# Optimization experiments

Hardware: AMD Instinct MI355X
Metric: run time of the kernel (lower is better)

## Reference

```python
import jax, jax.numpy as jnp
import numpy as np

NEG = -9999.0      # chart init / clip floor (np.clip a_min=-9999.0)
THRESH = -9000.0   # 'pseudo_score > -9000' acceptance gate
ARC_BONUS = 5.0    # '+ 5' added to every arc candidate


def _fill_chart(vinfo):
    """Eisner DP chart fill, faithful to the sequential numpy triple loop.
    vinfo: [N, N] arc scores. Returns (score_chart [N,N,2,2], backtrace [N,N,2,2]).
    Chart axes: [i, j, direction, completeness] as in the torch source.
    Parallelized over span start i and split q; sequential over width k via scan.
    Sequential-update subtleties of the original q-loop are reproduced exactly:
      * complete (0,1) at q=i reads the (0,0) cell as it stands after only the
        q=i incomplete update ('part00');
      * complete (1,1) at q=j reads the fully updated (1,0) cell ('new10');
      * complete (0,1) at q=j and (1,1) at q=i are strict-improvement no-ops;
      * ties keep the earliest q (jnp.argmax returns first occurrence).
    """
    N = vinfo.shape[0]
    idx = jnp.arange(N)
    ii = idx[:, None]   # span start i
    mm = idx[None, :]   # split offset m; q = i + m
    S = jnp.full((N, N, 2, 2), NEG, dtype=vinfo.dtype).at[idx, idx].set(0.0)
    BT = jnp.zeros((N, N, 2, 2), dtype=jnp.int32)

    def step(carry, k):
        S, BT = carry
        j = idx + k
        row_ok = j < N
        okb = row_ok[:, None]
        jc = jnp.minimum(j, N - 1)
        jb = jc[:, None]
        q = ii + mm
        qc = jnp.minimum(q, N - 1)
        q1c = jnp.minimum(q + 1, N - 1)

        # ---- incomplete spans (0,0) and (1,0): q in [i, j-1]  <=>  m in [0, k-1]
        base = jnp.where((mm < k) & okb,
                         S[:, :, 1, 1][ii, qc] + S[:, :, 0, 1][q1c, jb],
                         -jnp.inf)                      # [N (i), N (m)]
        vL = vinfo[jc, idx][:, None]   # vinfo[j, i] -> arc j<-...: head j
        vR = vinfo[idx, jc][:, None]   # vinfo[i, j]
        p00 = jnp.maximum(base + vL + ARC_BONUS, NEG)
        p10 = jnp.maximum(base + vR + ARC_BONUS, NEG)
        m00 = jnp.max(p00, axis=1); q00 = idx + jnp.argmax(p00, axis=1)
        m10 = jnp.max(p10, axis=1); q10 = idx + jnp.argmax(p10, axis=1)
        ok00 = row_ok & (m00 > THRESH)
        ok10 = row_ok & (m10 > THRESH)
        # chart[i,j,0,0] as it stands right after the q=i iteration
        part00 = jnp.where(row_ok & (p00[:, 0] > THRESH), p00[:, 0], NEG)
        new10 = jnp.where(ok10, m10, NEG)

        m_mid = (mm >= 1) & (mm < k) & okb
        # ---- complete (0,1): q=i uses partially built (0,0); q=j is a no-op
        c01 = jnp.where(m_mid, S[:, :, 0, 1][ii, qc] + S[:, :, 0, 0][qc, jb], -jnp.inf)
        c01 = c01.at[:, 0].set(jnp.where(row_ok, part00, -jnp.inf))
        p01 = jnp.maximum(c01, NEG)
        m01 = jnp.max(p01, axis=1); q01 = idx + jnp.argmax(p01, axis=1)
        ok01 = row_ok & (m01 > THRESH)

        # ---- complete (1,1): q=i is a no-op; q=j uses freshly updated (1,0)
        c11 = jnp.where(m_mid, S[:, :, 1, 0][ii, qc] + S[:, :, 1, 1][qc, jb], -jnp.inf)
        c11 = jnp.where((mm == k) & okb, new10[:, None], c11)
        p11 = jnp.maximum(c11, NEG)
        m11 = jnp.max(p11, axis=1); q11 = idx + jnp.argmax(p11, axis=1)
        ok11 = row_ok & (m11 > THRESH)

        def upd(S, BT, a, b, ok, val, qarg):
            S = S.at[idx, jc, a, b].set(jnp.where(ok, val, S[idx, jc, a, b]))
            BT = BT.at[idx, jc, a, b].set(
                jnp.where(ok, qarg, BT[idx, jc, a, b]).astype(jnp.int32))
            return S, BT

        S, BT = upd(S, BT, 0, 0, ok00, m00, q00)
        S, BT = upd(S, BT, 1, 0, ok10, m10, q10)
        S, BT = upd(S, BT, 0, 1, ok01, m01, q01)
        S, BT = upd(S, BT, 1, 1, ok11, m11, q11)
        return (S, BT), None

    (S, BT), _ = jax.lax.scan(step, (S, BT), jnp.arange(1, N))
    return S, BT


def setup_inputs() -> dict:
    key = jax.random.key(0)
    B, N = 64, 128
    b_vinfo_mtx = jax.random.normal(key, (B, N, N), dtype=jnp.float32)
    b_buffer_size = jnp.full((B,), N, dtype=jnp.int32)
    return {"b_vinfo_mtx": b_vinfo_mtx, "b_buffer_size": b_buffer_size}


def reference(b_vinfo_mtx, b_buffer_size):
    # All sentences use the full buffer (b_buffer_size == N), so the batch is
    # processed as one vmapped chart fill.
    scores, backtrace = jax.vmap(_fill_chart)(b_vinfo_mtx)
    return scores, backtrace
```

## Files before the change

kernel.cpp:

```cpp
#include <hip/hip_runtime.h>
#include <stdint.h>

static constexpr int kN = 128;
static constexpr int kTri = (kN * (kN - 1)) / 2;
static constexpr int kTriD = (kN * (kN + 1)) / 2;
static constexpr int kThreads = 1024;
static constexpr float kNeg = -9999.0f;
static constexpr float kThresh = -9000.0f;
static constexpr float kArcBonus = 5.0f;
static constexpr int kDynLds = kTriD * 16;
static constexpr int kCMax = 9;

__device__ __forceinline__ int rowBase(int i) { return (i * (2 * kN - 1 - i)) / 2; }
__device__ __forceinline__ int colBaseD(int c) { return (c * (c + 1)) / 2; }

__device__ __forceinline__ void ldsBarrier() {
    asm volatile("s_waitcnt lgkmcnt(0)\n\ts_barrier" ::: "memory");
}

template <int CTRL>
__device__ __forceinline__ float dppMax(float x) {
    const int y = __builtin_amdgcn_update_dpp(__float_as_int(x), __float_as_int(x),
                                              CTRL, 0xF, 0xF, true);
    return fmaxf(x, __int_as_float(y));
}
__device__ __forceinline__ float swzMax16(float x) {
    const int y = __builtin_amdgcn_ds_swizzle(__float_as_int(x), 0x401F);
    return fmaxf(x, __int_as_float(y));
}

__device__ __forceinline__ int lpOf(int k) {
    if (k <= 16) return 0;
    if (k < 64) return 3;
    if (k < 96) return 4;
    if (k < 112) return 5;
    return 6;
}
__device__ __forceinline__ void mapStatic(int nk, int tid, int& i, int& j, bool& act) {
    const int lp = lpOf(nk);
    i = tid >> lp;
    j = i + nk;
    act = i < (kN - nk);
}

__device__ __forceinline__ void scanChunk(const float4* __restrict__ Q4,
                                          int i, int j, int k, int mlo, int mhi,
                                          float vL,
                                          float& bmax, int& ib,
                                          float& v01, int& i01,
                                          float& v11, int& i11) {
    const int qjb = colBaseD(j);
    int q, mstart;
    float4 cur;
    if (mlo == 0) {
        q = i + 1;
        cur = Q4[qjb + q];
        bmax = cur.z; ib = 0;
        const float p00 = (cur.z + vL) + kArcBonus;
        v01 = (p00 > kThresh) ? p00 : kNeg; i01 = 0;
        mstart = 1;
    } else {
        q = i + mlo;
        cur = Q4[qjb + q];
        mstart = mlo;
    }
    int dA = colBaseD(q) + i;
    int dInc = q + 1;
#pragma unroll 8
    for (int m = mstart; m < mhi; ++m) {
        const float4 nxt = Q4[qjb + q + 1];
        const float4 diq = Q4[dA];
        const float base = diq.y + nxt.z;
        const float p01 = diq.z + cur.x;
        const float p11 = diq.w + cur.y;
        if (base > bmax) { bmax = base; ib = m; }
        if (p01 > v01) { v01 = p01; i01 = m; }
        if (p11 > v11) { v11 = p11; i11 = m; }
        cur = nxt;
        dA += dInc; ++dInc;
        ++q;
    }
}

__device__ __forceinline__ void writeCell(float4* __restrict__ Q4,
                                          uint32_t* __restrict__ wsBT,
                                          int i, int j, int k,
                                          float gb, int ib, float vLc, float vRc,
                                          float v01, int i01, float v11, int i11) {
    const float v00 = (gb + vLc) + kArcBonus;
    const float v10 = (gb + vRc) + kArcBonus;
    const float new10 = (v10 > kThresh) ? v10 : kNeg;
    if (new10 > v11) { v11 = new10; i11 = k; }
    float4 w = make_float4(kNeg, kNeg, kNeg, kNeg);
    uint32_t p = 0;
    if (v00 > kThresh) { w.x = v00; p |= (uint32_t)(i + ib); }
    if (v01 > kThresh) { w.z = v01; p |= (uint32_t)(i + i01) << 8; }
    if (v10 > kThresh) { w.w = v10; p |= (uint32_t)(i + ib) << 16; }
    if (v11 > kThresh) { w.y = v11; p |= (uint32_t)(i + i11) << 24; }
    Q4[colBaseD(j) + i] = w;
    wsBT[rowBase(i) + k - 1] = p;
}

__device__ __forceinline__ void doStepSerial(int k, int tid,
                                             float4* __restrict__ Q4,
                                             uint32_t* __restrict__ wsBT,
                                             const float* __restrict__ v,
                                             int& ci, int& cj, bool& cact,
                                             float& vL, float& vR) {
    const int i = ci, j = cj;
    const bool act = cact;
    const float vLc = vL, vRc = vR;
    float bmax = -3.0e38f, v01 = -3.0e38f, v11 = -3.0e38f;
    int ib = 0, i01 = 0, i11 = 0x7FFFFFFF;
    if (act) {
        scanChunk(Q4, i, j, k, 0, k, vLc, bmax, ib, v01, i01, v11, i11);
    }
    if (k + 1 < kN) {
        mapStatic(k + 1, tid, ci, cj, cact);
        vL = cact ? v[cj * kN + ci] : 0.f;
        vR = cact ? v[ci * kN + cj] : 0.f;
    }
    if (act) {
        writeCell(Q4, wsBT, i, j, k, bmax, ib, vLc, vRc, v01, i01, v11, i11);
    }
}

template <int LP, int C>
__device__ __forceinline__ void preloadRow(int k0, int tid,
                                           const float4* __restrict__ Q4,
                                           float (&r11)[kCMax], float (&r01)[kCMax],
                                           float (&r10)[kCMax]) {
    constexpr int P = 1 << LP;
    const int i = tid >> LP;
    const int l = tid & (P - 1);
    const int mlo = l * C;
    const int mstart = mlo ? mlo : 1;
    const bool act = i < (kN - k0);
#pragma unroll
    for (int c = 0; c < C; ++c) {
        const int m = mstart + c;
        if (act && (m < mlo + C) && (m <= k0 - 2)) {
            const float4 d = Q4[colBaseD(i + m) + i];
            r11[c] = d.y; r01[c] = d.z; r10[c] = d.w;
        }
    }
}

template <int LP, int C>
__device__ __forceinline__ void doStepC(int k, int tid, int laneId,
                                        float4* __restrict__ Q4,
                                        uint32_t* __restrict__ wsBT,
                                        const float* __restrict__ v,
                                        int& ci, int& cj, bool& cact,
                                        float& vL, float& vR,
                                        float (&r11)[kCMax], float (&r01)[kCMax],
                                        float (&r10)[kCMax]) {
    constexpr int P = 1 << LP;
    const int i = ci, j = cj;
    const bool act = cact;
    const float vLc = vL, vRc = vR;
    const int l = tid & (P - 1);
    const int mlo = l * C;
    const int mstart = mlo ? mlo : 1;
    const int mhi = (mlo + C < k) ? (mlo + C) : k;
    const bool waveActive = (((tid & ~63) >> LP) < (kN - k));

    float bmax = -3.0e38f, v01 = -3.0e38f, v11 = -3.0e38f;
    int ib = 0x7FFFFFFF, i01 = 0x7FFFFFFF, i11 = 0x7FFFFFFF;

    const int mf = k - 1;
    float4 fresh = make_float4(kNeg, kNeg, kNeg, kNeg);
    if (act && (mf >= mstart) && (mf < mlo + C)) {
        fresh = Q4[colBaseD(i + mf) + i];
    }

    const bool lact = waveActive && act && (mstart < mhi);
    const int qjb = colBaseD(j);
    float4 cur = make_float4(0.f, 0.f, 0.f, 0.f);
    if (lact) cur = Q4[qjb + i + mstart];
    if (act && mlo == 0) {
        bmax = cur.z; ib = 0;
        const float p00 = (cur.z + vLc) + kArcBonus;
        v01 = (p00 > kThresh) ? p00 : kNeg; i01 = 0;
    }
#pragma unroll
    for (int c = 0; c < C; ++c) {
        const int m = mstart + c;
        const bool isF = (m == mf);
        const float a11 = isF ? fresh.y : r11[c];
        const float a01 = isF ? fresh.z : r01[c];
        const float a10 = isF ? fresh.w : r10[c];
        r11[c] = a11; r01[c] = a01; r10[c] = a10;
        const bool on = lact && (m < mhi);
        if (on) {
            const float4 nxt = Q4[qjb + i + m + 1];
            const float base = a11 + nxt.z;
            const float p01v = a01 + cur.x;
            const float p11v = a10 + cur.y;
            if (base > bmax) { bmax = base; ib = m; }
            if (p01v > v01) { v01 = p01v; i01 = m; }
            if (p11v > v11) { v11 = p11v; i11 = m; }
            cur = nxt;
        }
    }

    if (k + 1 < kN) {
        mapStatic(k + 1, tid, ci, cj, cact);
        vL = cact ? v[cj * kN + ci] : 0.f;
        vR = cact ? v[ci * kN + cj] : 0.f;
    }

    if (waveActive) {
        float gB = dppMax<0x141>(dppMax<0x4E>(dppMax<0xB1>(bmax)));
        float g01 = dppMax<0x141>(dppMax<0x4E>(dppMax<0xB1>(v01)));
        float g11 = dppMax<0x141>(dppMax<0x4E>(dppMax<0xB1>(v11)));
        if constexpr (P >= 16) {
            gB = dppMax<0x140>(gB); g01 = dppMax<0x140>(g01); g11 = dppMax<0x140>(g11);
        }
        if constexpr (P >= 32) {
            gB = swzMax16(gB); g01 = swzMax16(g01); g11 = swzMax16(g11);
        }
        if constexpr (P == 64) {
            gB = fmaxf(gB, __shfl_xor(gB, 32, 64));
            g01 = fmaxf(g01, __shfl_xor(g01, 32, 64));
            g11 = fmaxf(g11, __shfl_xor(g11, 32, 64));
        }
        const int grpStart = laneId & ~(P - 1);
        const uint64_t gmask =
            (P == 64) ? ~0ull : (((1ull << P) - 1ull) << grpStart);
        const uint64_t mB = __ballot(bmax == gB) & gmask;
        const uint64_t m2 = __ballot(v01 == g01) & gmask;
        const uint64_t m3 = __ballot(v11 == g11) & gmask;
        const int rB = __shfl(ib, __ffsll((unsigned long long)mB) - 1, 64);
        const int rq01 = __shfl(i01, __ffsll((unsigned long long)m2) - 1, 64);
        const int rq11 = __shfl(i11, __ffsll((unsigned long long)m3) - 1, 64);
        if (act && l == 0) {
            writeCell(Q4, wsBT, i, j, k, gB, rB, vLc, vRc, g01, rq01, g11, rq11);
        }
    }
}

__global__ __launch_bounds__(kThreads) void eisner_dp(
    const float* __restrict__ vinfo,
    float* __restrict__ outS,
    float* __restrict__ outBT,
    uint32_t* __restrict__ btPacked)
{
    extern __shared__ float4 Q4[];

    const int tid = threadIdx.x;
    const int laneId = tid & 63;
    const int b = blockIdx.x;
    const float* v = vinfo + (size_t)b * kN * kN;
    uint32_t* wsBT = btPacked + (size_t)b * kTri;

    const float4 zeroq = make_float4(0.f, 0.f, 0.f, 0.f);
    if (tid < kN) Q4[colBaseD(tid) + tid] = zeroq;

    float r11[kCMax], r01[kCMax], r10[kCMax];
#pragma unroll
    for (int c = 0; c < kCMax; ++c) { r11[c] = kNeg; r01[c] = kNeg; r10[c] = kNeg; }

    int ci, cj; bool cact;
    mapStatic(1, tid, ci, cj, cact);
    float vL = cact ? v[cj * kN + ci] : 0.f;
    float vR = cact ? v[ci * kN + cj] : 0.f;
    __syncthreads();

    for (int k = 1; k <= 16; ++k) {
        doStepSerial(k, tid, Q4, wsBT, v, ci, cj, cact, vL, vR);
        ldsBarrier();
    }
    preloadRow<3, 5>(17, tid, Q4, r11, r01, r10);
    for (int k = 17; k < 40; ++k) {
        doStepC<3, 5>(k, tid, laneId, Q4, wsBT, v, ci, cj, cact, vL, vR, r11, r01, r10);
        ldsBarrier();
    }
    preloadRow<3, 9>(40, tid, Q4, r11, r01, r10);
    for (int k = 40; k < 64; ++k) {
        doStepC<3, 9>(k, tid, laneId, Q4, wsBT, v, ci, cj, cact, vL, vR, r11, r01, r10);
        ldsBarrier();
    }
    preloadRow<4, 7>(64, tid, Q4, r11, r01, r10);
    for (int k = 64; k < 96; ++k) {
        doStepC<4, 7>(k, tid, laneId, Q4, wsBT, v, ci, cj, cact, vL, vR, r11, r01, r10);
        ldsBarrier();
    }
    preloadRow<5, 5>(96, tid, Q4, r11, r01, r10);
    for (int k = 96; k < 112; ++k) {
        doStepC<5, 5>(k, tid, laneId, Q4, wsBT, v, ci, cj, cact, vL, vR, r11, r01, r10);
        ldsBarrier();
    }
    preloadRow<6, 3>(112, tid, Q4, r11, r01, r10);
    for (int k = 112; k < 128; ++k) {
        doStepC<6, 3>(k, tid, laneId, Q4, wsBT, v, ci, cj, cact, vL, vR, r11, r01, r10);
        ldsBarrier();
    }

    __syncthreads();

    float4* gS4 = (float4*)(outS + (size_t)b * kN * kN * 4);
    float4* gB4 = (float4*)(outBT + (size_t)b * kN * kN * 4);
    const float4 negq = make_float4(kNeg, kNeg, kNeg, kNeg);
    for (int c = tid; c < kN * kN; c += kThreads) {
        const int i = c >> 7, j = c & (kN - 1);
        if (i < j) {
            const float4 q = Q4[colBaseD(j) + i];
            gS4[c] = make_float4(q.x, q.z, q.w, q.y);
            const uint32_t p = wsBT[rowBase(i) + (j - i - 1)];
            gB4[c] = make_float4((float)(p & 255u), (float)((p >> 8) & 255u),
                                 (float)((p >> 16) & 255u), (float)(p >> 24));
        } else if (i == j) {
            gS4[c] = zeroq;
            gB4[c] = zeroq;
        } else {
            gS4[c] = negq;
            gB4[c] = zeroq;
        }
    }
}

extern "C" void kernel_launch(void* const* d_in, const int* in_sizes, int n_in,
                              void* d_out, int out_size, void* d_ws, size_t ws_size,
                              hipStream_t stream) {
    (void)n_in; (void)out_size; (void)ws_size;
    const float* vinfo = (const float*)d_in[0];
    const int B = in_sizes[1];
    float* outS = (float*)d_out;
    float* outBT = outS + (size_t)B * kN * kN * 4;
    uint32_t* btPacked = (uint32_t*)d_ws;

    hipFuncSetAttribute(reinterpret_cast<const void*>(eisner_dp),
                        hipFuncAttributeMaxDynamicSharedMemorySize, kDynLds);

    eisner_dp<<<dim3(B), dim3(kThreads), kDynLds, stream>>>(vinfo, outS, outBT, btPacked);
}
```

Baseline: 258.7 us.

## Prefetch next-step column entries and forward fresh cell values in registers

Each thread now loads the LDS column entries it needs for step k+1 before the barrier of step k, and keeps its freshly reduced cell values (after threshold and clip) in registers instead of rereading them from LDS. The one entry that depends on the current step's writes (m=1 / col[0] for lane-group start) is loaded after the barrier, and its comparison is deferred and applied with tie-aware ordering. The aim is to take LDS load latency off the critical path between barriers. In exchange it adds register pressure (up to 10 float4 per thread), and the deferred tie-breaking logic is delicate.

```diff
diff --git a/kernel.cpp b/kernel.cpp
--- a/kernel.cpp
+++ b/kernel.cpp
@@ -139,10 +139,44 @@
 #pragma unroll
     for (int c = 0; c < C; ++c) {
         const int m = mstart + c;
-        if (act && (m < mlo + C) && (m <= k0 - 2)) {
+        if (act && (m < mlo + C) && (m <= k0 - 1)) {
             const float4 d = Q4[colBaseD(i + m) + i];
             r11[c] = d.y; r01[c] = d.z; r10[c] = d.w;
         }
+    }
+}
+
+template <int LP, int C>
+__device__ __forceinline__ void fwInit(int k0, int tid,
+                                       const float (&r11)[kCMax], const float (&r01)[kCMax],
+                                       const float (&r10)[kCMax],
+                                       float& fw11, float& fw01, float& fw10) {
+    constexpr int P = 1 << LP;
+    const int l = tid & (P - 1);
+    const int mlo = l * C;
+    const int mstart = mlo ? mlo : 1;
+#pragma unroll
+    for (int c = 0; c < C; ++c) {
+        if (mstart + c == k0 - 1) { fw11 = r11[c]; fw01 = r01[c]; fw10 = r10[c]; }
+    }
+}
+
+template <int LP, int C>
+__device__ __forceinline__ void prefetchColEntry(int k, int tid,
+                                                 const float4* __restrict__ Q4,
+                                                 float4 (&col)[kCMax + 1]) {
+    constexpr int P = 1 << LP;
+    const int i = tid >> LP;
+    const int l = tid & (P - 1);
+    const int mlo = l * C;
+    const int mstart = mlo ? mlo : 1;
+    const bool act = i < (kN - k);
+    const int qjb = colBaseD(i + k);
+#pragma unroll
+    for (int c = 0; c <= C; ++c) {
+        int addr = qjb + i + mstart + c;
+        if (addr > kTriD - 1) addr = kTriD - 1;
+        if (act) col[c] = Q4[addr];
     }
 }
 
@@ -154,7 +188,10 @@
                                         int& ci, int& cj, bool& cact,
                                         float& vL, float& vR,
                                         float (&r11)[kCMax], float (&r01)[kCMax],
-                                        float (&r10)[kCMax]) {
+                                        float (&r10)[kCMax],
+                                        float4 (&col)[kCMax + 1],
+                                        float& fw11, float& fw01, float& fw10,
+                                        bool c0valid, bool prefetchNext) {
     constexpr int P = 1 << LP;
     const int i = ci, j = cj;
     const bool act = cact;
@@ -164,50 +201,71 @@
     const int mstart = mlo ? mlo : 1;
     const int mhi = (mlo + C < k) ? (mlo + C) : k;
     const bool waveActive = (((tid & ~63) >> LP) < (kN - k));
+    const int qjb = colBaseD(j);
+    const int mf = k - 1;
+
+    if (!c0valid) {
+        if (l == 0 && act) col[0] = Q4[qjb + i + 1];
+    }
 
     float bmax = -3.0e38f, v01 = -3.0e38f, v11 = -3.0e38f;
     int ib = 0x7FFFFFFF, i01 = 0x7FFFFFFF, i11 = 0x7FFFFFFF;
 
-    const int mf = k - 1;
-    float4 fresh = make_float4(kNeg, kNeg, kNeg, kNeg);
-    if (act && (mf >= mstart) && (mf < mlo + C)) {
-        fresh = Q4[colBaseD(i + mf) + i];
-    }
-
     const bool lact = waveActive && act && (mstart < mhi);
-    const int qjb = colBaseD(j);
-    float4 cur = make_float4(0.f, 0.f, 0.f, 0.f);
-    if (lact) cur = Q4[qjb + i + mstart];
-    if (act && mlo == 0) {
-        bmax = cur.z; ib = 0;
-        const float p00 = (cur.z + vLc) + kArcBonus;
+
+    if (c0valid && act && mlo == 0) {
+        bmax = col[0].z; ib = 0;
+        const float p00 = (col[0].z + vLc) + kArcBonus;
         v01 = (p00 > kThresh) ? p00 : kNeg; i01 = 0;
     }
+    const bool deferM1 = (!c0valid) && (mlo == 0);
 #pragma unroll
     for (int c = 0; c < C; ++c) {
         const int m = mstart + c;
         const bool isF = (m == mf);
-        const float a11 = isF ? fresh.y : r11[c];
-        const float a01 = isF ? fresh.z : r01[c];
-        const float a10 = isF ? fresh.w : r10[c];
+        const float a11 = isF ? fw11 : r11[c];
+        const float a01 = isF ? fw01 : r01[c];
+        const float a10 = isF ? fw10 : r10[c];
         r11[c] = a11; r01[c] = a01; r10[c] = a10;
-        const bool on = lact && (m < mhi);
+        const bool on = lact && (m < mhi) && !(deferM1 && c == 0);
         if (on) {
-            const float4 nxt = Q4[qjb + i + m + 1];
-            const float base = a11 + nxt.z;
-            const float p01v = a01 + cur.x;
-            const float p11v = a10 + cur.y;
+            const float base = a11 + col[c + 1].z;
+            const float p01v = a01 + col[c].x;
+            const float p11v = a10 + col[c].y;
             if (base > bmax) { bmax = base; ib = m; }
             if (p01v > v01) { v01 = p01v; i01 = m; }
             if (p11v > v11) { v11 = p11v; i11 = m; }
-            cur = nxt;
-        }
+        }
+    }
+    if (deferM1 && act) {
+        const float base1 = r11[0] + col[1].z;
+        if (base1 >= bmax) { bmax = base1; ib = 1; }
+        const float p011 = r01[0] + col[0].x;
+        if (p011 >= v01) { v01 = p011; i01 = 1; }
+        const float p111 = r10[0] + col[0].y;
+        if (p111 >= v11) { v11 = p111; i11 = 1; }
+        const float sb = col[0].z;
+        if (sb >= bmax) { bmax = sb; ib = 0; }
+        const float p00 = (sb + vLc) + kArcBonus;
+        const float sp = (p00 > kThresh) ? p00 : kNeg;
+        if (sp >= v01) { v01 = sp; i01 = 0; }
     }
 
     if (k + 1 < kN) {
         mapStatic(k + 1, tid, ci, cj, cact);
         vL = cact ? v[cj * kN + ci] : 0.f;
         vR = cact ? v[ci * kN + cj] : 0.f;
+    }
+
+    if (prefetchNext) {
+        const int qjb2 = qjb + j + 1;
+#pragma unroll
+        for (int c = 0; c <= C; ++c) {
+            const bool skip = (mlo == 0 && c == 0);
+            int addr = qjb2 + i + mstart + c;
+            if (addr > kTriD - 1) addr = kTriD - 1;
+            if (cact && !skip) col[c] = Q4[addr];
+        }
     }
 
     if (waveActive) {
@@ -234,6 +292,16 @@
         const int rB = __shfl(ib, __ffsll((unsigned long long)mB) - 1, 64);
         const int rq01 = __shfl(i01, __ffsll((unsigned long long)m2) - 1, 64);
         const int rq11 = __shfl(i11, __ffsll((unsigned long long)m3) - 1, 64);
+
+        const float v00f = (gB + vLc) + kArcBonus;
+        const float v10f = (gB + vRc) + kArcBonus;
+        const float new10 = (v10f > kThresh) ? v10f : kNeg;
+        float v11m = g11;
+        if (new10 > v11m) v11m = new10;
+        fw11 = (v11m > kThresh) ? v11m : kNeg;
+        fw01 = (g01 > kThresh) ? g01 : kNeg;
+        fw10 = (v10f > kThresh) ? v10f : kNeg;
+
         if (act && l == 0) {
             writeCell(Q4, wsBT, i, j, k, gB, rB, vLc, vRc, g01, rq01, g11, rq11);
         }
@@ -258,8 +326,12 @@
     if (tid < kN) Q4[colBaseD(tid) + tid] = zeroq;
 
     float r11[kCMax], r01[kCMax], r10[kCMax];
+    float4 col[kCMax + 1];
+    float fw11 = kNeg, fw01 = kNeg, fw10 = kNeg;
 #pragma unroll
     for (int c = 0; c < kCMax; ++c) { r11[c] = kNeg; r01[c] = kNeg; r10[c] = kNeg; }
+#pragma unroll
+    for (int c = 0; c <= kCMax; ++c) col[c] = zeroq;
 
     int ci, cj; bool cact;
     mapStatic(1, tid, ci, cj, cact);
@@ -272,28 +344,43 @@
         ldsBarrier();
     }
     preloadRow<3, 5>(17, tid, Q4, r11, r01, r10);
+    fwInit<3, 5>(17, tid, r11, r01, r10, fw11, fw01, fw10);
+    prefetchColEntry<3, 5>(17, tid, Q4, col);
     for (int k = 17; k < 40; ++k) {
-        doStepC<3, 5>(k, tid, laneId, Q4, wsBT, v, ci, cj, cact, vL, vR, r11, r01, r10);
+        doStepC<3, 5>(k, tid, laneId, Q4, wsBT, v, ci, cj, cact, vL, vR,
+                      r11, r01, r10, col, fw11, fw01, fw10, k == 17, k + 1 < 40);
         ldsBarrier();
     }
     preloadRow<3, 9>(40, tid, Q4, r11, r01, r10);
+    fwInit<3, 9>(40, tid, r11, r01, r10, fw11, fw01, fw10);
+    prefetchColEntry<3, 9>(40, tid, Q4, col);
     for (int k = 40; k < 64; ++k) {
-        doStepC<3, 9>(k, tid, laneId, Q4, wsBT, v, ci, cj, cact, vL, vR, r11, r01, r10);
+        doStepC<3, 9>(k, tid, laneId, Q4, wsBT, v, ci, cj, cact, vL, vR,
+                      r11, r01, r10, col, fw11, fw01, fw10, k == 40, k + 1 < 64);
         ldsBarrier();
     }
     preloadRow<4, 7>(64, tid, Q4, r11, r01, r10);
+    fwInit<4, 7>(64, tid, r11, r01, r10, fw11, fw01, fw10);
+    prefetchColEntry<4, 7>(64, tid, Q4, col);
     for (int k = 64; k < 96; ++k) {
-        doStepC<4, 7>(k, tid, laneId, Q4, wsBT, v, ci, cj, cact, vL, vR, r11, r01, r10);
+        doStepC<4, 7>(k, tid, laneId, Q4, wsBT, v, ci, cj, cact, vL, vR,
+                      r11, r01, r10, col, fw11, fw01, fw10, k == 64, k + 1 < 96);
         ldsBarrier();
     }
     preloadRow<5, 5>(96, tid, Q4, r11, r01, r10);
+    fwInit<5, 5>(96, tid, r11, r01, r10, fw11, fw01, fw10);
+    prefetchColEntry<5, 5>(96, tid, Q4, col);
     for (int k = 96; k < 112; ++k) {
-        doStepC<5, 5>(k, tid, laneId, Q4, wsBT, v, ci, cj, cact, vL, vR, r11, r01, r10);
+        doStepC<5, 5>(k, tid, laneId, Q4, wsBT, v, ci, cj, cact, vL, vR,
+                      r11, r01, r10, col, fw11, fw01, fw10, k == 96, k + 1 < 112);
         ldsBarrier();
     }
     preloadRow<6, 3>(112, tid, Q4, r11, r01, r10);
+    fwInit<6, 3>(112, tid, r11, r01, r10, fw11, fw01, fw10);
+    prefetchColEntry<6, 3>(112, tid, Q4, col);
     for (int k = 112; k < 128; ++k) {
-        doStepC<6, 3>(k, tid, laneId, Q4, wsBT, v, ci, cj, cact, vL, vR, r11, r01, r10);
+        doStepC<6, 3>(k, tid, laneId, Q4, wsBT, v, ci, cj, cact, vL, vR,
+                      r11, r01, r10, col, fw11, fw01, fw10, k == 112, k + 1 < 128);
         ldsBarrier();
     }
 
```

After: 277.4 us. 7.2% more time.

## Keep freshly computed diagonal chart cells in registers instead of reloading from LDS

Applied to the files above, without the earlier changes.

In the first 16 serial steps, each thread now keeps its own row's completed cells in a fully unrolled register array instead of re-reading the diagonal operand from LDS. In the chunked phase, the newest cell (m = k-1) is rebuilt in every lane from the wave-reduced maxima rather than loaded back from LDS, and the preload bound is widened to cover it. The goal is fewer dependent LDS loads on the serial critical path. The cost is more register pressure, with 51 extra floats per thread in the serial phase at 1024 threads per block, and some duplicated arithmetic in every lane.

```diff
diff --git a/kernel.cpp b/kernel.cpp
--- a/kernel.cpp
+++ b/kernel.cpp
@@ -43,50 +43,11 @@
     act = i < (kN - nk);
 }
 
-__device__ __forceinline__ void scanChunk(const float4* __restrict__ Q4,
-                                          int i, int j, int k, int mlo, int mhi,
-                                          float vL,
-                                          float& bmax, int& ib,
-                                          float& v01, int& i01,
-                                          float& v11, int& i11) {
-    const int qjb = colBaseD(j);
-    int q, mstart;
-    float4 cur;
-    if (mlo == 0) {
-        q = i + 1;
-        cur = Q4[qjb + q];
-        bmax = cur.z; ib = 0;
-        const float p00 = (cur.z + vL) + kArcBonus;
-        v01 = (p00 > kThresh) ? p00 : kNeg; i01 = 0;
-        mstart = 1;
-    } else {
-        q = i + mlo;
-        cur = Q4[qjb + q];
-        mstart = mlo;
-    }
-    int dA = colBaseD(q) + i;
-    int dInc = q + 1;
-#pragma unroll 8
-    for (int m = mstart; m < mhi; ++m) {
-        const float4 nxt = Q4[qjb + q + 1];
-        const float4 diq = Q4[dA];
-        const float base = diq.y + nxt.z;
-        const float p01 = diq.z + cur.x;
-        const float p11 = diq.w + cur.y;
-        if (base > bmax) { bmax = base; ib = m; }
-        if (p01 > v01) { v01 = p01; i01 = m; }
-        if (p11 > v11) { v11 = p11; i11 = m; }
-        cur = nxt;
-        dA += dInc; ++dInc;
-        ++q;
-    }
-}
-
-__device__ __forceinline__ void writeCell(float4* __restrict__ Q4,
-                                          uint32_t* __restrict__ wsBT,
-                                          int i, int j, int k,
-                                          float gb, int ib, float vLc, float vRc,
-                                          float v01, int i01, float v11, int i11) {
+__device__ __forceinline__ float4 writeCell(float4* __restrict__ Q4,
+                                            uint32_t* __restrict__ wsBT,
+                                            int i, int j, int k,
+                                            float gb, int ib, float vLc, float vRc,
+                                            float v01, int i01, float v11, int i11) {
     const float v00 = (gb + vLc) + kArcBonus;
     const float v10 = (gb + vRc) + kArcBonus;
     const float new10 = (v10 > kThresh) ? v10 : kNeg;
@@ -99,21 +60,41 @@
     if (v11 > kThresh) { w.y = v11; p |= (uint32_t)(i + i11) << 24; }
     Q4[colBaseD(j) + i] = w;
     wsBT[rowBase(i) + k - 1] = p;
-}
-
-__device__ __forceinline__ void doStepSerial(int k, int tid,
-                                             float4* __restrict__ Q4,
-                                             uint32_t* __restrict__ wsBT,
-                                             const float* __restrict__ v,
-                                             int& ci, int& cj, bool& cact,
-                                             float& vL, float& vR) {
+    return w;
+}
+
+__device__ __forceinline__ void doStepSerialReg(int k, int tid,
+                                                float4* __restrict__ Q4,
+                                                uint32_t* __restrict__ wsBT,
+                                                const float* __restrict__ v,
+                                                int& ci, int& cj, bool& cact,
+                                                float& vL, float& vR,
+                                                float (&sr11)[17], float (&sr01)[17],
+                                                float (&sr10)[17]) {
     const int i = ci, j = cj;
     const bool act = cact;
     const float vLc = vL, vRc = vR;
     float bmax = -3.0e38f, v01 = -3.0e38f, v11 = -3.0e38f;
     int ib = 0, i01 = 0, i11 = 0x7FFFFFFF;
     if (act) {
-        scanChunk(Q4, i, j, k, 0, k, vLc, bmax, ib, v01, i01, v11, i11);
+        const int qjb = colBaseD(j);
+        float4 cur = Q4[qjb + i + 1];
+        bmax = cur.z; ib = 0;
+        const float p00 = (cur.z + vLc) + kArcBonus;
+        v01 = (p00 > kThresh) ? p00 : kNeg; i01 = 0;
+#pragma unroll
+        for (int m = 1; m < 16; ++m) {
+            if (m < k) {
+                const float4 nxt = Q4[qjb + i + m + 1];
+                const float base = sr11[m] + nxt.z;
+                const float p01v = sr01[m] + cur.x;
+                const float p11v = sr10[m] + cur.y;
+                if (base > bmax) { bmax = base; ib = m; }
+                if (p01v > v01) { v01 = p01v; i01 = m; }
+                if (p11v > v11) { v11 = p11v; i11 = m; }
+                cur = nxt;
+            }
+        }
     }
     if (k + 1 < kN) {
         mapStatic(k + 1, tid, ci, cj, cact);
@@ -121,7 +102,9 @@
         vR = cact ? v[ci * kN + cj] : 0.f;
     }
     if (act) {
-        writeCell(Q4, wsBT, i, j, k, bmax, ib, vLc, vRc, v01, i01, v11, i11);
+        const float4 w = writeCell(Q4, wsBT, i, j, k, bmax, ib, vLc, vRc,
+                                   v01, i01, v11, i11);
+        sr11[k] = w.y; sr01[k] = w.z; sr10[k] = w.w;
     }
 }
 
@@ -139,10 +122,25 @@
 #pragma unroll
     for (int c = 0; c < C; ++c) {
         const int m = mstart + c;
-        if (act && (m < mlo + C) && (m <= k0 - 2)) {
+        if (act && (m < mlo + C) && (m <= k0 - 1)) {
             const float4 d = Q4[colBaseD(i + m) + i];
             r11[c] = d.y; r01[c] = d.z; r10[c] = d.w;
         }
+    }
+}
+
+template <int LP, int C>
+__device__ __forceinline__ void fwInit(int k0, int tid,
+                                       const float (&r11)[kCMax], const float (&r01)[kCMax],
+                                       const float (&r10)[kCMax],
+                                       float& fw11, float& fw01, float& fw10) {
+    constexpr int P = 1 << LP;
+    const int l = tid & (P - 1);
+    const int mlo = l * C;
+    const int mstart = mlo ? mlo : 1;
+#pragma unroll
+    for (int c = 0; c < C; ++c) {
+        if (mstart + c == k0 - 1) { fw11 = r11[c]; fw01 = r01[c]; fw10 = r10[c]; }
     }
 }
 
@@ -154,7 +152,8 @@
                                         int& ci, int& cj, bool& cact,
                                         float& vL, float& vR,
                                         float (&r11)[kCMax], float (&r01)[kCMax],
-                                        float (&r10)[kCMax]) {
+                                        float (&r10)[kCMax],
+                                        float& fw11, float& fw01, float& fw10) {
     constexpr int P = 1 << LP;
     const int i = ci, j = cj;
     const bool act = cact;
@@ -169,11 +168,6 @@
     int ib = 0x7FFFFFFF, i01 = 0x7FFFFFFF, i11 = 0x7FFFFFFF;
 
     const int mf = k - 1;
-    float4 fresh = make_float4(kNeg, kNeg, kNeg, kNeg);
-    if (act && (mf >= mstart) && (mf < mlo + C)) {
-        fresh = Q4[colBaseD(i + mf) + i];
-    }
-
     const bool lact = waveActive && act && (mstart < mhi);
     const int qjb = colBaseD(j);
     float4 cur = make_float4(0.f, 0.f, 0.f, 0.f);
@@ -187,9 +181,9 @@
     for (int c = 0; c < C; ++c) {
         const int m = mstart + c;
         const bool isF = (m == mf);
-        const float a11 = isF ? fresh.y : r11[c];
-        const float a01 = isF ? fresh.z : r01[c];
-        const float a10 = isF ? fresh.w : r10[c];
+        const float a11 = isF ? fw11 : r11[c];
+        const float a01 = isF ? fw01 : r01[c];
+        const float a10 = isF ? fw10 : r10[c];
         r11[c] = a11; r01[c] = a01; r10[c] = a10;
         const bool on = lact && (m < mhi);
         if (on) {
@@ -234,6 +228,17 @@
         const int rB = __shfl(ib, __ffsll((unsigned long long)mB) - 1, 64);
         const int rq01 = __shfl(i01, __ffsll((unsigned long long)m2) - 1, 64);
         const int rq11 = __shfl(i11, __ffsll((unsigned long long)m3) - 1, 64);
+
+        const float v00f = (gB + vLc) + kArcBonus;
+        const float v10f = (gB + vRc) + kArcBonus;
+        const float new10 = (v10f > kThresh) ? v10f : kNeg;
+        float v11m = g11;
+        if (new10 > v11m) v11m = new10;
+        fw11 = (v11m > kThresh) ? v11m : kNeg;
+        fw01 = (g01 > kThresh) ? g01 : kNeg;
+        fw10 = (v10f > kThresh) ? v10f : kNeg;
+        (void)v00f;
+
         if (act && l == 0) {
             writeCell(Q4, wsBT, i, j, k, gB, rB, vLc, vRc, g01, rq01, g11, rq11);
         }
@@ -257,43 +262,60 @@
     const float4 zeroq = make_float4(0.f, 0.f, 0.f, 0.f);
     if (tid < kN) Q4[colBaseD(tid) + tid] = zeroq;
 
-    float r11[kCMax], r01[kCMax], r10[kCMax];
-#pragma unroll
-    for (int c = 0; c < kCMax; ++c) { r11[c] = kNeg; r01[c] = kNeg; r10[c] = kNeg; }
-
     int ci, cj; bool cact;
     mapStatic(1, tid, ci, cj, cact);
     float vL = cact ? v[cj * kN + ci] : 0.f;
     float vR = cact ? v[ci * kN + cj] : 0.f;
     __syncthreads();
 
-    for (int k = 1; k <= 16; ++k) {
-        doStepSerial(k, tid, Q4, wsBT, v, ci, cj, cact, vL, vR);
-        ldsBarrier();
-    }
+    {
+        float sr11[17], sr01[17], sr10[17];
+#pragma unroll
+        for (int k = 1; k <= 16; ++k) {
+            doStepSerialReg(k, tid, Q4, wsBT, v, ci, cj, cact, vL, vR,
+                            sr11, sr01, sr10);
+            ldsBarrier();
+        }
+    }
+
+    float r11[kCMax], r01[kCMax], r10[kCMax];
+    float fw11 = kNeg, fw01 = kNeg, fw10 = kNeg;
+#pragma unroll
+    for (int c = 0; c < kCMax; ++c) { r11[c] = kNeg; r01[c] = kNeg; r10[c] = kNeg; }
+
     preloadRow<3, 5>(17, tid, Q4, r11, r01, r10);
+    fwInit<3, 5>(17, tid, r11, r01, r10, fw11, fw01, fw10);
     for (int k = 17; k < 40; ++k) {
-        doStepC<3, 5>(k, tid, laneId, Q4, wsBT, v, ci, cj, cact, vL, vR, r11, r01, r10);
+        doStepC<3, 5>(k, tid, laneId, Q4, wsBT, v, ci, cj, cact, vL, vR,
+                      r11, r01, r10, fw11, fw01, fw10);
         ldsBarrier();
     }
     preloadRow<3, 9>(40, tid, Q4, r11, r01, r10);
+    fwInit<3, 9>(40, tid, r11, r01, r10, fw11, fw01, fw10);
     for (int k = 40; k < 64; ++k) {
-        doStepC<3, 9>(k, tid, laneId, Q4, wsBT, v, ci, cj, cact, vL, vR, r11, r01, r10);
+        doStepC<3, 9>(k, tid, laneId, Q4, wsBT, v, ci, cj, cact, vL, vR,
+                      r11, r01, r10, fw11, fw01, fw10);
         ldsBarrier();
     }
     preloadRow<4, 7>(64, tid, Q4, r11, r01, r10);
+    fwInit<4, 7>(64, tid, r11, r01, r10, fw11, fw01, fw10);
     for (int k = 64; k < 96; ++k) {
-        doStepC<4, 7>(k, tid, laneId, Q4, wsBT, v, ci, cj, cact, vL, vR, r11, r01, r10);
+        doStepC<4, 7>(k, tid, laneId, Q4, wsBT, v, ci, cj, cact, vL, vR,
+                      r11, r01, r10, fw11, fw01, fw10);
         ldsBarrier();
     }
     preloadRow<5, 5>(96, tid, Q4, r11, r01, r10);
+    fwInit<5, 5>(96, tid, r11, r01, r10, fw11, fw01, fw10);
     for (int k = 96; k < 112; ++k) {
-        doStepC<5, 5>(k, tid, laneId, Q4, wsBT, v, ci, cj, cact, vL, vR, r11, r01, r10);
+        doStepC<5, 5>(k, tid, laneId, Q4, wsBT, v, ci, cj, cact, vL, vR,
+                      r11, r01, r10, fw11, fw01, fw10);
         ldsBarrier();
     }
     preloadRow<6, 3>(112, tid, Q4, r11, r01, r10);
+    fwInit<6, 3>(112, tid, r11, r01, r10, fw11, fw01, fw10);
     for (int k = 112; k < 128; ++k) {
-        doStepC<6, 3>(k, tid, laneId, Q4, wsBT, v, ci, cj, cact, vL, vR, r11, r01, r10);
+        doStepC<6, 3>(k, tid, laneId, Q4, wsBT, v, ci, cj, cact, vL, vR,
+                      r11, r01, r10, fw11, fw01, fw10);
         ldsBarrier();
     }
 
```

Measured after the change: 244.9 us. -5.3%, faster.
